# Kernel tuning notes

Hardware: AMD Instinct MI355X
Metric: run time of the kernel (lower is better)

The kernel has to match this reference:

```python
import jax, jax.numpy as jnp
import numpy as np


def _pool_mat(n_in, n_out):
    # AdaptiveAvgPool1d(n_out) over a length-n_in axis, as a dense [n_out, n_in] averaging matrix.
    M = np.zeros((n_out, n_in), dtype=np.float32)
    for i in range(n_out):
        s = (i * n_in) // n_out
        e = -(-((i + 1) * n_in) // n_out)  # ceil
        M[i, s:e] = 1.0 / (e - s)
    return M


def _ln(x, g, b, eps=1e-5):
    m = jnp.mean(x, axis=-1, keepdims=True)
    xc = x - m
    v = jnp.mean(xc * xc, axis=-1, keepdims=True)
    return xc * jax.lax.rsqrt(v + eps) * g + b


def setup_inputs():
    T, TOK, P, N, D, L, C = 16, 16384, 8192, 32768, 128, 8, 16
    key = jax.random.key(0)
    ks = jax.random.split(key, 9)
    x = jax.random.normal(ks[0], (T, TOK, D), dtype=jnp.float32)
    # P node-token positions per timestamp (models padded_node_mask with P True entries)
    node_pos = jnp.sort(jax.vmap(lambda k: jax.random.permutation(k, TOK)[:P])(jax.random.split(ks[1], T)), axis=1).astype(jnp.int32)
    # unique entire-graph node ids per timestamp (scatter destinations)
    node_ids = jax.vmap(lambda k: jax.random.permutation(k, N)[:P])(jax.random.split(ks[2], T)).astype(jnp.int32)
    g_enc = 1.0 + 0.1 * jax.random.normal(ks[3], (D,), dtype=jnp.float32)
    b_enc = 0.1 * jax.random.normal(ks[4], (D,), dtype=jnp.float32)
    g_fin = 1.0 + 0.1 * jax.random.normal(ks[5], (L * C,), dtype=jnp.float32)
    b_fin = 0.1 * jax.random.normal(ks[6], (L * C,), dtype=jnp.float32)
    g_dec = 1.0 + 0.1 * jax.random.normal(ks[7], (C,), dtype=jnp.float32)
    b_dec = 0.1 * jax.random.normal(ks[8], (C,), dtype=jnp.float32)
    return {"x": x, "g_enc": g_enc, "b_enc": b_enc, "g_fin": g_fin, "b_fin": b_fin,
            "g_dec": g_dec, "b_dec": b_dec, "node_pos": node_pos, "node_ids": node_ids,
            "num_nodes": N}


def reference(x, g_enc, b_enc, g_fin, b_fin, g_dec, b_dec, node_pos, node_ids, num_nodes):
    T, TOK, D = x.shape
    C = g_dec.shape[0]
    L = g_fin.shape[0] // C
    N = int(num_nodes)
    # ---- encode ----
    xn = _ln(x, g_enc, b_enc)                                   # encode_layer_norm
    nodes = jnp.take_along_axis(xn, node_pos[:, :, None], axis=1)  # masked gather [T,P,D]
    # _to_entire: scatter node embeddings into zero [T,N,D]
    tee = jnp.zeros((T, N, D), x.dtype).at[jnp.arange(T)[:, None], node_ids].set(nodes)
    A1 = jnp.asarray(_pool_mat(D, C))                            # AdaptiveAvgPool1d(comp_dim)
    pooled = jnp.einsum('tnd,cd->tnc', tee, A1)                  # [T,N,C]
    groups = np.array_split(np.arange(N), L)
    max_len = max(len(g) for g in groups)
    stacked = np.stack([np.pad(g, (0, max_len - len(g))) for g in groups])  # [L,max_len]
    grouped = jnp.take(pooled, jnp.asarray(stacked), axis=1)     # [T,L,max_len,C]
    comp = (grouped.sum(axis=2) / max_len).reshape(T, 1, L * C)  # segment mean-pool
    comp = _ln(comp, g_fin, b_fin)                               # encode_final_layer_norm
    # ---- decode ----
    vals = jnp.broadcast_to(comp.reshape(T, L, 1, C), (T, L, max_len, C)).reshape(T, L * max_len, C)
    tee2 = jnp.zeros((T, N, C), x.dtype).at[:, jnp.asarray(stacked.reshape(-1)), :].set(vals)
    dn = _ln(tee2, g_dec, b_dec)                                 # decode_norm
    A2 = jnp.asarray(_pool_mat(C, D))                            # AdaptiveAvgPool1d(embed_dim)
    out = jnp.einsum('tnc,dc->tnd', dn, A2)                      # [T,N,D]
    return out
```

## Files before the change

### kernel.cpp

```cpp
#include <hip/hip_runtime.h>

#define T_   16
#define TOK_ 16384
#define P_   8192
#define N_   32768
#define D_   128
#define L_   8
#define C_   16

typedef float f32x2 __attribute__((ext_vector_type(2)));
typedef float f32x4 __attribute__((ext_vector_type(4)));

constexpr int K1_BLOCKS     = 2048;
constexpr int BLOCKS_PER_T  = 128;
constexpr int ROWS_PER_WAVE = 16;

__global__ __launch_bounds__(256) void k1_gather_ln_pool(
    const float* __restrict__ x,
    const float* __restrict__ g_enc, const float* __restrict__ b_enc,
    const int* __restrict__ node_pos, const int* __restrict__ node_ids,
    float* __restrict__ partial)
{
    __shared__ float lds[4 * 128];
    const int tid   = threadIdx.x;
    const int lane  = tid & 63;
    const int wid   = tid >> 6;
    const int j     = lane & 15;
    const int q     = lane >> 4;
    const int b     = blockIdx.x;
    const int t     = b >> 7;
    const int chunk = b & 127;
    const int pbase = chunk * 64 + wid * ROWS_PER_WAVE;
    const int tP    = t * P_;
    const float* xt = x + (size_t)t * TOK_ * D_;

    const f32x4 g0 = *(const f32x4*)(g_enc + 8 * j);
    const f32x4 g1 = *(const f32x4*)(g_enc + 8 * j + 4);
    const f32x4 bb0 = *(const f32x4*)(b_enc + 8 * j);
    const f32x4 bb1 = *(const f32x4*)(b_enc + 8 * j + 4);
    const float G = g0.x + g0.y + g0.z + g0.w + g1.x + g1.y + g1.z + g1.w;
    const float B = bb0.x + bb0.y + bb0.z + bb0.w + bb1.x + bb1.y + bb1.z + bb1.w;

    const int posv = node_pos[tP + pbase + j];
    const int nidv = node_ids[tP + pbase + j];

    f32x4 va[4], vb[4];
#pragma unroll
    for (int i = 0; i < 4; ++i) {
        const int p = __shfl(posv, i * 4 + q);
        const float* row = xt + (size_t)p * D_ + 8 * j;
        va[i] = *(const f32x4*)(row);
        vb[i] = *(const f32x4*)(row + 4);
    }

    float acc[L_];
#pragma unroll
    for (int ll = 0; ll < L_; ++ll) acc[ll] = 0.f;

#pragma unroll
    for (int i = 0; i < 4; ++i) {
        const f32x4 a = va[i], c = vb[i];
        float s  = a.x + a.y + a.z + a.w + c.x + c.y + c.z + c.w;
        float ss = a.x*a.x + a.y*a.y + a.z*a.z + a.w*a.w
                 + c.x*c.x + c.y*c.y + c.z*c.z + c.w*c.w;
        float dot = a.x*g0.x + a.y*g0.y + a.z*g0.z + a.w*g0.w
                  + c.x*g1.x + c.y*g1.y + c.z*g1.z + c.w*g1.w;
#pragma unroll
        for (int m = 1; m < 16; m <<= 1) {
            s  += __shfl_xor(s, m);
            ss += __shfl_xor(ss, m);
        }
        const float mean = s * (1.f / 128.f);
        const float rstd = rsqrtf(ss * (1.f / 128.f) - mean * mean + 1e-5f);
        const float srow = (dot - mean * G) * rstd + B;
        const int l = __shfl(nidv, i * 4 + q) >> 12;
#pragma unroll
        for (int ll = 0; ll < L_; ++ll) acc[ll] += (ll == l) ? srow : 0.f;
    }

#pragma unroll
    for (int ll = 0; ll < L_; ++ll) {
        acc[ll] += __shfl_xor(acc[ll], 16);
        acc[ll] += __shfl_xor(acc[ll], 32);
    }
    if (lane < 16) {
#pragma unroll
        for (int ll = 0; ll < L_; ++ll) lds[wid * 128 + ll * 16 + j] = acc[ll];
    }
    __syncthreads();
    if (tid < 128) {
        const float sum = lds[tid] + lds[128 + tid] + lds[256 + tid] + lds[384 + tid];
        partial[(size_t)b * 128 + tid] = sum;
    }
}

__global__ __launch_bounds__(64) void k2_finalize(
    const float* __restrict__ partial,
    const float* __restrict__ g_fin, const float* __restrict__ b_fin,
    const float* __restrict__ g_dec, const float* __restrict__ b_dec,
    float* __restrict__ decoded)
{
    const int t = blockIdx.x;
    const int lane = threadIdx.x;
    const float* pb = partial + (size_t)t * BLOCKS_PER_T * 128;
    float a0 = 0.f, a1 = 0.f;
#pragma unroll 8
    for (int k = 0; k < BLOCKS_PER_T; ++k) {
        a0 += pb[k * 128 + lane];
        a1 += pb[k * 128 + 64 + lane];
    }
    a0 *= (1.f / 32768.f);
    a1 *= (1.f / 32768.f);

    float s = a0 + a1, ss = a0 * a0 + a1 * a1;
#pragma unroll
    for (int m = 1; m < 64; m <<= 1) {
        s  += __shfl_xor(s, m);
        ss += __shfl_xor(ss, m);
    }
    const float mean = s * (1.f / 128.f);
    const float rstd = rsqrtf(ss * (1.f / 128.f) - mean * mean + 1e-5f);
    const float c0 = (a0 - mean) * rstd * g_fin[lane]      + b_fin[lane];
    const float c1 = (a1 - mean) * rstd * g_fin[lane + 64] + b_fin[lane + 64];

    float s0 = c0, q0 = c0 * c0, s1 = c1, q1 = c1 * c1;
#pragma unroll
    for (int m = 1; m < 16; m <<= 1) {
        s0 += __shfl_xor(s0, m); q0 += __shfl_xor(q0, m);
        s1 += __shfl_xor(s1, m); q1 += __shfl_xor(q1, m);
    }
    const float m0 = s0 * (1.f / 16.f), m1 = s1 * (1.f / 16.f);
    const float r0 = rsqrtf(q0 * (1.f / 16.f) - m0 * m0 + 1e-5f);
    const float r1 = rsqrtf(q1 * (1.f / 16.f) - m1 * m1 + 1e-5f);
    const int c = lane & 15;
    const float gd = g_dec[c], bd = b_dec[c];
    decoded[t * 128 + lane]      = (c0 - m0) * r0 * gd + bd;
    decoded[t * 128 + 64 + lane] = (c1 - m1) * r1 * gd + bd;
}

__global__ __launch_bounds__(256) void k3_broadcast(
    const float* __restrict__ decoded, f32x4* __restrict__ out)
{
    const int tid   = threadIdx.x;
    const int b     = blockIdx.x;
    const int t     = b >> 7;
    const int chunk = b & 127;
    const int l     = chunk >> 4;
    const float val = decoded[(t << 7) + (l << 4) + ((tid & 31) >> 1)];
    const f32x4 v4 = {val, val, val, val};
    f32x4* p = out + (((size_t)t << 20) + ((size_t)chunk << 13) + tid);
#pragma unroll
    for (int it = 0; it < 32; ++it)
        __builtin_nontemporal_store(v4, p + (it << 8));
}

extern "C" void kernel_launch(void* const* d_in, const int* in_sizes, int n_in,
                              void* d_out, int out_size, void* d_ws, size_t ws_size,
                              hipStream_t stream)
{
    const float* x      = (const float*)d_in[0];
    const float* g_enc  = (const float*)d_in[1];
    const float* b_enc  = (const float*)d_in[2];
    const float* g_fin  = (const float*)d_in[3];
    const float* b_fin  = (const float*)d_in[4];
    const float* g_dec  = (const float*)d_in[5];
    const float* b_dec  = (const float*)d_in[6];
    const int*   node_pos = (const int*)d_in[7];
    const int*   node_ids = (const int*)d_in[8];

    float* partial = (float*)d_ws;
    float* decoded = partial + (size_t)K1_BLOCKS * 128;
    float* out = (float*)d_out;

    hipLaunchKernelGGL(k1_gather_ln_pool, dim3(K1_BLOCKS), dim3(256), 0, stream,
                       x, g_enc, b_enc, node_pos, node_ids, partial);
    hipLaunchKernelGGL(k2_finalize, dim3(T_), dim3(64), 0, stream,
                       partial, g_fin, b_fin, g_dec, b_dec, decoded);
    hipLaunchKernelGGL(k3_broadcast, dim3(2048), dim3(256), 0, stream,
                       decoded, (f32x4*)out);
}
```

Before: 72.69 us.

## Fuse gather-LN-pool, finalize and broadcast into one cooperative kernel with grid sync

Replaces three kernel launches with one cooperative kernel of 1024 blocks that uses a grid-wide sync between the partial-reduction phase and the finalize/broadcast phase. Each block now processes 128 rows in two passes, and each block redundantly computes the per-timestamp finalize from 64 partials into shared memory before writing its slice of the output. This removes launch gaps and the separate tiny finalize kernel. In exchange it adds grid-sync cost, caps occupancy to co-resident blocks, and switches the output stores from nontemporal to regular stores.

```diff
diff --git a/kernel.cpp b/kernel.cpp
--- a/kernel.cpp
+++ b/kernel.cpp
@@ -1,4 +1,7 @@
 #include <hip/hip_runtime.h>
+#include <hip/hip_cooperative_groups.h>
+
+namespace cg = cooperative_groups;
 
 #define T_   16
 #define TOK_ 16384
@@ -8,150 +11,153 @@
 #define L_   8
 #define C_   16
 
-typedef float f32x2 __attribute__((ext_vector_type(2)));
 typedef float f32x4 __attribute__((ext_vector_type(4)));
 
-constexpr int K1_BLOCKS     = 2048;
-constexpr int BLOCKS_PER_T  = 128;
-constexpr int ROWS_PER_WAVE = 16;
+constexpr int NBLOCKS      = 1024;
+constexpr int BLOCKS_PER_T = 64;
+constexpr int ROWS_PER_BLK = 128;
 
-__global__ __launch_bounds__(256) void k1_gather_ln_pool(
+__global__ __launch_bounds__(256, 4) void fused_all(
     const float* __restrict__ x,
     const float* __restrict__ g_enc, const float* __restrict__ b_enc,
+    const float* __restrict__ g_fin, const float* __restrict__ b_fin,
+    const float* __restrict__ g_dec, const float* __restrict__ b_dec,
     const int* __restrict__ node_pos, const int* __restrict__ node_ids,
-    float* __restrict__ partial)
+    float* __restrict__ partial, float* __restrict__ out)
 {
     __shared__ float lds[4 * 128];
+    __shared__ float dec[128];
     const int tid   = threadIdx.x;
     const int lane  = tid & 63;
     const int wid   = tid >> 6;
     const int j     = lane & 15;
     const int q     = lane >> 4;
     const int b     = blockIdx.x;
-    const int t     = b >> 7;
-    const int chunk = b & 127;
-    const int pbase = chunk * 64 + wid * ROWS_PER_WAVE;
+    const int t     = b >> 6;
+    const int chunk = b & 63;
     const int tP    = t * P_;
     const float* xt = x + (size_t)t * TOK_ * D_;
 
-    const f32x4 g0 = *(const f32x4*)(g_enc + 8 * j);
-    const f32x4 g1 = *(const f32x4*)(g_enc + 8 * j + 4);
-    const f32x4 bb0 = *(const f32x4*)(b_enc + 8 * j);
-    const f32x4 bb1 = *(const f32x4*)(b_enc + 8 * j + 4);
-    const float G = g0.x + g0.y + g0.z + g0.w + g1.x + g1.y + g1.z + g1.w;
-    const float B = bb0.x + bb0.y + bb0.z + bb0.w + bb1.x + bb1.y + bb1.z + bb1.w;
+    {
+        const f32x4 g0  = *(const f32x4*)(g_enc + 8 * j);
+        const f32x4 g1  = *(const f32x4*)(g_enc + 8 * j + 4);
+        const f32x4 bb0 = *(const f32x4*)(b_enc + 8 * j);
+        const f32x4 bb1 = *(const f32x4*)(b_enc + 8 * j + 4);
+        const float G = g0.x + g0.y + g0.z + g0.w + g1.x + g1.y + g1.z + g1.w;
+        const float B = bb0.x + bb0.y + bb0.z + bb0.w + bb1.x + bb1.y + bb1.z + bb1.w;
 
-    const int posv = node_pos[tP + pbase + j];
-    const int nidv = node_ids[tP + pbase + j];
+        float acc[L_];
+#pragma unroll
+        for (int ll = 0; ll < L_; ++ll) acc[ll] = 0.f;
 
-    f32x4 va[4], vb[4];
 #pragma unroll
-    for (int i = 0; i < 4; ++i) {
-        const int p = __shfl(posv, i * 4 + q);
-        const float* row = xt + (size_t)p * D_ + 8 * j;
-        va[i] = *(const f32x4*)(row);
-        vb[i] = *(const f32x4*)(row + 4);
+        for (int pass = 0; pass < 2; ++pass) {
+            const int pbase = chunk * ROWS_PER_BLK + pass * 64 + wid * 16;
+            const int posv = node_pos[tP + pbase + j];
+            const int nidv = node_ids[tP + pbase + j];
+
+            f32x4 va[4], vb[4];
+#pragma unroll
+            for (int i = 0; i < 4; ++i) {
+                const int p = __shfl(posv, i * 4 + q);
+                const float* row = xt + (size_t)p * D_ + 8 * j;
+                va[i] = *(const f32x4*)(row);
+                vb[i] = *(const f32x4*)(row + 4);
+            }
+#pragma unroll
+            for (int i = 0; i < 4; ++i) {
+                const f32x4 a = va[i], c = vb[i];
+                float s  = a.x + a.y + a.z + a.w + c.x + c.y + c.z + c.w;
+                float ss = a.x*a.x + a.y*a.y + a.z*a.z + a.w*a.w
+                         + c.x*c.x + c.y*c.y + c.z*c.z + c.w*c.w;
+                float dot = a.x*g0.x + a.y*g0.y + a.z*g0.z + a.w*g0.w
+                          + c.x*g1.x + c.y*g1.y + c.z*g1.z + c.w*g1.w;
+#pragma unroll
+                for (int m = 1; m < 16; m <<= 1) {
+                    s  += __shfl_xor(s, m);
+                    ss += __shfl_xor(ss, m);
+                }
+                const float mean = s * (1.f / 128.f);
+                const float rstd = rsqrtf(ss * (1.f / 128.f) - mean * mean + 1e-5f);
+                const float srow = (dot - mean * G) * rstd + B;
+                const int l = __shfl(nidv, i * 4 + q) >> 12;
+#pragma unroll
+                for (int ll = 0; ll < L_; ++ll) acc[ll] += (ll == l) ? srow : 0.f;
+            }
+        }
+
+#pragma unroll
+        for (int ll = 0; ll < L_; ++ll) {
+            acc[ll] += __shfl_xor(acc[ll], 16);
+            acc[ll] += __shfl_xor(acc[ll], 32);
+        }
+        if (lane < 16) {
+#pragma unroll
+            for (int ll = 0; ll < L_; ++ll) lds[wid * 128 + ll * 16 + j] = acc[ll];
+        }
+        __syncthreads();
+        if (tid < 128) {
+            const float sum = lds[tid] + lds[128 + tid] + lds[256 + tid] + lds[384 + tid];
+            partial[(size_t)b * 128 + tid] = sum;
+        }
     }
 
-    float acc[L_];
+    cg::this_grid().sync();
+
+    {
+        const float* pb = partial + (size_t)t * BLOCKS_PER_T * 128;
+        float a0 = 0.f, a1 = 0.f;
+        const int k0 = wid * 16;
+#pragma unroll 4
+        for (int k = 0; k < 16; ++k) {
+            a0 += pb[(k0 + k) * 128 + lane];
+            a1 += pb[(k0 + k) * 128 + 64 + lane];
+        }
+        lds[wid * 128 + lane]      = a0;
+        lds[wid * 128 + 64 + lane] = a1;
+        __syncthreads();
+        if (wid == 0) {
+            float c0 = (lds[lane] + lds[128 + lane] + lds[256 + lane] + lds[384 + lane])
+                       * (1.f / 32768.f);
+            float c1 = (lds[64 + lane] + lds[192 + lane] + lds[320 + lane] + lds[448 + lane])
+                       * (1.f / 32768.f);
+            float s = c0 + c1, ss = c0 * c0 + c1 * c1;
 #pragma unroll
-    for (int ll = 0; ll < L_; ++ll) acc[ll] = 0.f;
+            for (int m = 1; m < 64; m <<= 1) {
+                s  += __shfl_xor(s, m);
+                ss += __shfl_xor(ss, m);
+            }
+            const float mean = s * (1.f / 128.f);
+            const float rstd = rsqrtf(ss * (1.f / 128.f) - mean * mean + 1e-5f);
+            const float e0 = (c0 - mean) * rstd * g_fin[lane]      + b_fin[lane];
+            const float e1 = (c1 - mean) * rstd * g_fin[lane + 64] + b_fin[lane + 64];
 
+            float s0 = e0, q0 = e0 * e0, s1 = e1, q1 = e1 * e1;
 #pragma unroll
-    for (int i = 0; i < 4; ++i) {
-        const f32x4 a = va[i], c = vb[i];
-        float s  = a.x + a.y + a.z + a.w + c.x + c.y + c.z + c.w;
-        float ss = a.x*a.x + a.y*a.y + a.z*a.z + a.w*a.w
-                 + c.x*c.x + c.y*c.y + c.z*c.z + c.w*c.w;
-        float dot = a.x*g0.x + a.y*g0.y + a.z*g0.z + a.w*g0.w
-                  + c.x*g1.x + c.y*g1.y + c.z*g1.z + c.w*g1.w;
-#pragma unroll
-        for (int m = 1; m < 16; m <<= 1) {
-            s  += __shfl_xor(s, m);
-            ss += __shfl_xor(ss, m);
+            for (int m = 1; m < 16; m <<= 1) {
+                s0 += __shfl_xor(s0, m); q0 += __shfl_xor(q0, m);
+                s1 += __shfl_xor(s1, m); q1 += __shfl_xor(q1, m);
+            }
+            const float m0 = s0 * (1.f / 16.f), m1 = s1 * (1.f / 16.f);
+            const float r0 = rsqrtf(q0 * (1.f / 16.f) - m0 * m0 + 1e-5f);
+            const float r1 = rsqrtf(q1 * (1.f / 16.f) - m1 * m1 + 1e-5f);
+            const int c = lane & 15;
+            const float gd = g_dec[c], bd = b_dec[c];
+            dec[lane]      = (e0 - m0) * r0 * gd + bd;
+            dec[64 + lane] = (e1 - m1) * r1 * gd + bd;
         }
-        const float mean = s * (1.f / 128.f);
-        const float rstd = rsqrtf(ss * (1.f / 128.f) - mean * mean + 1e-5f);
-        const float srow = (dot - mean * G) * rstd + B;
-        const int l = __shfl(nidv, i * 4 + q) >> 12;
-#pragma unroll
-        for (int ll = 0; ll < L_; ++ll) acc[ll] += (ll == l) ? srow : 0.f;
+        __syncthreads();
     }
 
+    {
+        const int s = chunk;
+        const float val = dec[((s >> 3) << 4) + ((tid & 31) >> 1)];
+        const f32x4 v4 = {val, val, val, val};
+        f32x4* p = (f32x4*)out + (((size_t)t << 20) + ((size_t)s << 14) + tid);
 #pragma unroll
-    for (int ll = 0; ll < L_; ++ll) {
-        acc[ll] += __shfl_xor(acc[ll], 16);
-        acc[ll] += __shfl_xor(acc[ll], 32);
+        for (int it = 0; it < 64; ++it)
+            p[it * 256] = v4;
     }
-    if (lane < 16) {
-#pragma unroll
-        for (int ll = 0; ll < L_; ++ll) lds[wid * 128 + ll * 16 + j] = acc[ll];
-    }
-    __syncthreads();
-    if (tid < 128) {
-        const float sum = lds[tid] + lds[128 + tid] + lds[256 + tid] + lds[384 + tid];
-        partial[(size_t)b * 128 + tid] = sum;
-    }
-}
-
-__global__ __launch_bounds__(64) void k2_finalize(
-    const float* __restrict__ partial,
-    const float* __restrict__ g_fin, const float* __restrict__ b_fin,
-    const float* __restrict__ g_dec, const float* __restrict__ b_dec,
-    float* __restrict__ decoded)
-{
-    const int t = blockIdx.x;
-    const int lane = threadIdx.x;
-    const float* pb = partial + (size_t)t * BLOCKS_PER_T * 128;
-    float a0 = 0.f, a1 = 0.f;
-#pragma unroll 8
-    for (int k = 0; k < BLOCKS_PER_T; ++k) {
-        a0 += pb[k * 128 + lane];
-        a1 += pb[k * 128 + 64 + lane];
-    }
-    a0 *= (1.f / 32768.f);
-    a1 *= (1.f / 32768.f);
-
-    float s = a0 + a1, ss = a0 * a0 + a1 * a1;
-#pragma unroll
-    for (int m = 1; m < 64; m <<= 1) {
-        s  += __shfl_xor(s, m);
-        ss += __shfl_xor(ss, m);
-    }
-    const float mean = s * (1.f / 128.f);
-    const float rstd = rsqrtf(ss * (1.f / 128.f) - mean * mean + 1e-5f);
-    const float c0 = (a0 - mean) * rstd * g_fin[lane]      + b_fin[lane];
-    const float c1 = (a1 - mean) * rstd * g_fin[lane + 64] + b_fin[lane + 64];
-
-    float s0 = c0, q0 = c0 * c0, s1 = c1, q1 = c1 * c1;
-#pragma unroll
-    for (int m = 1; m < 16; m <<= 1) {
-        s0 += __shfl_xor(s0, m); q0 += __shfl_xor(q0, m);
-        s1 += __shfl_xor(s1, m); q1 += __shfl_xor(q1, m);
-    }
-    const float m0 = s0 * (1.f / 16.f), m1 = s1 * (1.f / 16.f);
-    const float r0 = rsqrtf(q0 * (1.f / 16.f) - m0 * m0 + 1e-5f);
-    const float r1 = rsqrtf(q1 * (1.f / 16.f) - m1 * m1 + 1e-5f);
-    const int c = lane & 15;
-    const float gd = g_dec[c], bd = b_dec[c];
-    decoded[t * 128 + lane]      = (c0 - m0) * r0 * gd + bd;
-    decoded[t * 128 + 64 + lane] = (c1 - m1) * r1 * gd + bd;
-}
-
-__global__ __launch_bounds__(256) void k3_broadcast(
-    const float* __restrict__ decoded, f32x4* __restrict__ out)
-{
-    const int tid   = threadIdx.x;
-    const int b     = blockIdx.x;
-    const int t     = b >> 7;
-    const int chunk = b & 127;
-    const int l     = chunk >> 4;
-    const float val = decoded[(t << 7) + (l << 4) + ((tid & 31) >> 1)];
-    const f32x4 v4 = {val, val, val, val};
-    f32x4* p = out + (((size_t)t << 20) + ((size_t)chunk << 13) + tid);
-#pragma unroll
-    for (int it = 0; it < 32; ++it)
-        __builtin_nontemporal_store(v4, p + (it << 8));
 }
 
 extern "C" void kernel_launch(void* const* d_in, const int* in_sizes, int n_in,
@@ -169,13 +175,13 @@
     const int*   node_ids = (const int*)d_in[8];
 
     float* partial = (float*)d_ws;
-    float* decoded = partial + (size_t)K1_BLOCKS * 128;
-    float* out = (float*)d_out;
+    float* out     = (float*)d_out;
 
-    hipLaunchKernelGGL(k1_gather_ln_pool, dim3(K1_BLOCKS), dim3(256), 0, stream,
-                       x, g_enc, b_enc, node_pos, node_ids, partial);
-    hipLaunchKernelGGL(k2_finalize, dim3(T_), dim3(64), 0, stream,
-                       partial, g_fin, b_fin, g_dec, b_dec, decoded);
-    hipLaunchKernelGGL(k3_broadcast, dim3(2048), dim3(256), 0, stream,
-                       decoded, (f32x4*)out);
+    void* args[] = {
+        (void*)&x, (void*)&g_enc, (void*)&b_enc, (void*)&g_fin, (void*)&b_fin,
+        (void*)&g_dec, (void*)&b_dec, (void*)&node_pos, (void*)&node_ids,
+        (void*)&partial, (void*)&out
+    };
+    hipLaunchCooperativeKernel((const void*)fused_all, dim3(NBLOCKS), dim3(256),
+                               args, 0, stream);
 }
```

Measured after the change: 177.8 us. 2.45x slower.
